# Performance work log

Measured on AMD Instinct MI355X. Metric: run time of the kernel, lower is better.

The kernel has to match this reference:

```python
import jax, jax.numpy as jnp
import numpy as np

VOCAB, D_IN, D_H = 32000, 512, 1024
B, T = 16, 256
PAD_IDX = 0


def setup_inputs() -> dict:
    key = jax.random.key(0)
    k1, k2, k3, k4, k5 = jax.random.split(key, 5)
    input_idx = jax.random.randint(k1, (B, T), 0, VOCAB, dtype=jnp.int64)
    emb = jax.random.normal(k2, (VOCAB, D_IN), dtype=jnp.float32) * 0.02
    emb = emb.at[PAD_IDX].set(0.0)  # padding_idx row is zero
    weight_x = jax.random.normal(k3, (D_H, D_IN), dtype=jnp.float32) * (1.0 / np.sqrt(D_IN))
    weight_h = jax.random.normal(k4, (D_H, D_H), dtype=jnp.float32) * (1.0 / np.sqrt(D_H))
    bias = jnp.zeros((D_H,), dtype=jnp.float32)
    lm_W = jax.random.normal(k5, (VOCAB, D_H), dtype=jnp.float32) * (1.0 / np.sqrt(D_H))
    return {"input_idx": input_idx, "emb": emb, "weight_x": weight_x,
            "weight_h": weight_h, "bias": bias, "lm_W": lm_W}


def reference(input_idx, emb, weight_x, weight_h, bias, lm_W):
    Bsz = input_idx.shape[0]
    h0 = jnp.zeros((Bsz, weight_h.shape[0]), dtype=weight_x.dtype)

    def step(h, tok):
        x = emb[tok]  # [B, D_IN]
        h_new = jnp.tanh(x @ weight_x.T + h @ weight_h.T + bias)
        mask = (tok != PAD_IDX)[:, None]  # keep old h at pad positions
        h = jnp.where(mask, h_new, h)
        return h, h

    _, h_all = jax.lax.scan(step, h0, input_idx.T)  # [T, B, H]
    h_all = jnp.swapaxes(h_all, 0, 1)               # [B, T, H]
    logits = jnp.einsum('bth,vh->btv', h_all, lm_W)  # [B, T, V]
    return logits
```

## Files before the change

### kernel.cpp

```cpp
#include <hip/hip_runtime.h>

#define PAD_IDX 0

typedef __attribute__((ext_vector_type(8))) short short8;
typedef __attribute__((ext_vector_type(4))) float f32x4;

__device__ __forceinline__ unsigned short f32_to_bf16_rne(float f) {
  unsigned int u = __builtin_bit_cast(unsigned int, f);
  u += 0x7FFFu + ((u >> 16) & 1u);
  return (unsigned short)(u >> 16);
}

__device__ __forceinline__ void load16_to_lds(const void* g, void* lds) {
  __builtin_amdgcn_global_load_lds(
      (const __attribute__((address_space(1))) unsigned int*)g,
      (__attribute__((address_space(3))) unsigned int*)lds,
      16, 0, 0);
}

__global__ void sentinel_kernel(float* out) { out[0] = 1.0e6f; }

__global__ __launch_bounds__(256) void cvt_kernel(const float* __restrict__ in,
                                                  unsigned short* __restrict__ out,
                                                  int n8) {
  int stride = gridDim.x * blockDim.x;
  for (int i = blockIdx.x * blockDim.x + threadIdx.x; i < n8; i += stride) {
    float4 a = ((const float4*)in)[2 * i];
    float4 b = ((const float4*)in)[2 * i + 1];
    ushort4 lo, hi;
    lo.x = f32_to_bf16_rne(a.x); lo.y = f32_to_bf16_rne(a.y);
    lo.z = f32_to_bf16_rne(a.z); lo.w = f32_to_bf16_rne(a.w);
    hi.x = f32_to_bf16_rne(b.x); hi.y = f32_to_bf16_rne(b.y);
    hi.z = f32_to_bf16_rne(b.z); hi.w = f32_to_bf16_rne(b.w);
    ((ushort4*)out)[2 * i] = lo;
    ((ushort4*)out)[2 * i + 1] = hi;
  }
}

__global__ __launch_bounds__(256) void xw_kernel(const int* __restrict__ tok,
                                                 const float* __restrict__ emb,
                                                 const float* __restrict__ Wx,
                                                 const float* __restrict__ bias,
                                                 float* __restrict__ xw) {
  __shared__ float At[32][68];
  __shared__ float Bt[32][68];
  __shared__ int stok[64];
  int tid = threadIdx.x;
  int tm = blockIdx.x & 63;
  int tn = blockIdx.x >> 6;
  int r0 = tm * 64, j0 = tn * 64;
  if (tid < 64) stok[tid] = tok[r0 + tid];
  int tx = tid & 15, ty = tid >> 4;
  float acc[4][4] = {};
  for (int kt = 0; kt < 512; kt += 32) {
    __syncthreads();
    #pragma unroll
    for (int ii = 0; ii < 2; ++ii) {
      int idx = tid * 2 + ii;
      int m = idx >> 3, fv = idx & 7;
      float4 va = *(const float4*)&emb[(size_t)stok[m] * 512 + kt + fv * 4];
      float4 vb = *(const float4*)&Wx[(size_t)(j0 + m) * 512 + kt + fv * 4];
      At[fv * 4 + 0][m] = va.x; At[fv * 4 + 1][m] = va.y;
      At[fv * 4 + 2][m] = va.z; At[fv * 4 + 3][m] = va.w;
      Bt[fv * 4 + 0][m] = vb.x; Bt[fv * 4 + 1][m] = vb.y;
      Bt[fv * 4 + 2][m] = vb.z; Bt[fv * 4 + 3][m] = vb.w;
    }
    __syncthreads();
    #pragma unroll
    for (int k = 0; k < 32; ++k) {
      float4 a4 = *(const float4*)&At[k][ty * 4];
      float4 b4 = *(const float4*)&Bt[k][tx * 4];
      float av[4] = {a4.x, a4.y, a4.z, a4.w};
      float bv[4] = {b4.x, b4.y, b4.z, b4.w};
      #pragma unroll
      for (int i = 0; i < 4; ++i)
        #pragma unroll
        for (int jj = 0; jj < 4; ++jj) acc[i][jj] = fmaf(av[i], bv[jj], acc[i][jj]);
    }
  }
  #pragma unroll
  for (int i = 0; i < 4; ++i) {
    size_t row = (size_t)(r0 + ty * 4 + i) * 1024 + j0 + tx * 4;
    #pragma unroll
    for (int jj = 0; jj < 4; ++jj)
      xw[row + jj] = acc[i][jj] + bias[j0 + tx * 4 + jj];
  }
}

__global__ __launch_bounds__(1024, 4) void rec_kernel(const float* __restrict__ Wh,
                                                      const float* __restrict__ xw,
                                                      const int* __restrict__ tok,
                                                      unsigned long long* hcomb,
                                                      unsigned short* __restrict__ h_all) {
  int c = blockIdx.x & 15;
  int g = blockIdx.x >> 4;
  int tid = threadIdx.x;
  int kk = tid & 15;
  int j = g * 64 + (tid >> 4);

  const float* wb = Wh + (size_t)j * 1024 + kk * 64;
#define LDW(i) f32x4 w##i = *(const f32x4*)(wb + i * 4);
  LDW(0) LDW(1) LDW(2) LDW(3) LDW(4) LDW(5) LDW(6) LDW(7)
  LDW(8) LDW(9) LDW(10) LDW(11) LDW(12) LDW(13) LDW(14) LDW(15)
#undef LDW

  __shared__ float hs[16 * 68];
  int lidx = (tid >> 6) * 68 + (tid & 63);
  unsigned long long* hc0 = hcomb + (size_t)c * 1024;
  unsigned long long* hc1 = hcomb + 16 * 1024 + (size_t)c * 1024;
  bool writer = (kk == 0);

  for (int t = 0; t < 256; ++t) {
    float xv = 0.f;
    int tkn = 1;
    if (writer) {
      xv = xw[((size_t)c * 256 + t) * 1024 + j];
      tkn = tok[c * 256 + t];
    }
    unsigned long long* src = ((t & 1) ? hc1 : hc0) + tid;
    unsigned long long v;
    int guard = 0;
    do {
      v = __hip_atomic_load(src, __ATOMIC_RELAXED, __HIP_MEMORY_SCOPE_AGENT);
      if ((unsigned int)(v >> 32) == (unsigned int)t) break;
      __builtin_amdgcn_s_sleep(1);
    } while (++guard < (1 << 20));
    hs[lidx] = __builtin_bit_cast(float, (unsigned int)v);
    __asm__ volatile("s_waitcnt lgkmcnt(0)\n\ts_barrier" ::: "memory");

    const float* hp = hs + kk * 68;
    f32x4 a0 = {0.f, 0.f, 0.f, 0.f}, a1 = a0, a2 = a0, a3 = a0;
#define FMAI(i, acc) { f32x4 h4 = *(const f32x4*)(hp + i * 4); acc += w##i * h4; }
    FMAI(0, a0) FMAI(1, a1) FMAI(2, a2) FMAI(3, a3)
    FMAI(4, a0) FMAI(5, a1) FMAI(6, a2) FMAI(7, a3)
    FMAI(8, a0) FMAI(9, a1) FMAI(10, a2) FMAI(11, a3)
    FMAI(12, a0) FMAI(13, a1) FMAI(14, a2) FMAI(15, a3)
#undef FMAI
    f32x4 aa = (a0 + a1) + (a2 + a3);
    float s = (aa[0] + aa[1]) + (aa[2] + aa[3]);
    s += __shfl_xor(s, 1);
    s += __shfl_xor(s, 2);
    s += __shfl_xor(s, 4);
    s += __shfl_xor(s, 8);

    if (writer) {
      float hnew;
      if (tkn != PAD_IDX) {
        float pre = xv + s;
        float e = __builtin_amdgcn_exp2f(pre * 2.8853900817779268f);
        hnew = 1.0f - 2.0f / (e + 1.0f);
      } else {
        hnew = hs[(j >> 6) * 68 + (j & 63)];
      }
      unsigned long long pv =
          ((unsigned long long)(unsigned int)(t + 1) << 32) |
          (unsigned long long)__builtin_bit_cast(unsigned int, hnew);
      __hip_atomic_store((((t + 1) & 1) ? hc1 : hc0) + j, pv,
                         __ATOMIC_RELAXED, __HIP_MEMORY_SCOPE_AGENT);
      h_all[((size_t)c * 256 + t) * 1024 + j] = f32_to_bf16_rne(hnew);
    }
    __asm__ volatile("s_waitcnt lgkmcnt(0)\n\ts_barrier" ::: "memory");
  }
}

__global__ __launch_bounds__(256) void gemm_kernel(const unsigned short* __restrict__ A,
                                                   const unsigned short* __restrict__ B,
                                                   float* __restrict__ C) {
  __shared__ unsigned short sA[128 * 64];
  __shared__ unsigned short sB[128 * 64];
  int tid = threadIdx.x;
  int lane = tid & 63, wave = tid >> 6;
  int id = blockIdx.x;
  int s = (id & 7) * 1000 + (id >> 3);
  int tm = s & 31, tn = s >> 5;
  int r0 = tm * 128, c0 = tn * 128;
  int wm = wave >> 1, wn = wave & 1;
  f32x4 zero = {0.f, 0.f, 0.f, 0.f};
  f32x4 acc[4][4];
  #pragma unroll
  for (int i = 0; i < 4; ++i)
    #pragma unroll
    for (int jx = 0; jx < 4; ++jx) acc[i][jx] = zero;

  for (int kt = 0; kt < 16; ++kt) {
    __syncthreads();
    #pragma unroll
    for (int i = 0; i < 4; ++i) {
      int slot = i * 256 + tid;
      int m = slot >> 3, sg = slot & 7;
      int kg = sg ^ (m & 7);
      const unsigned short* ga = A + (size_t)(r0 + m) * 1024 + kt * 64 + kg * 8;
      load16_to_lds(ga, &sA[(i * 256 + wave * 64) * 8]);
      const unsigned short* gb = B + (size_t)(c0 + m) * 1024 + kt * 64 + kg * 8;
      load16_to_lds(gb, &sB[(i * 256 + wave * 64) * 8]);
    }
    __syncthreads();
    #pragma unroll
    for (int kkb = 0; kkb < 2; ++kkb) {
      short8 af[4], bf[4];
      int kbyte = kkb * 64 + (lane >> 4) * 16;
      #pragma unroll
      for (int i = 0; i < 4; ++i) {
        int row = wm * 64 + i * 16 + (lane & 15);
        int off = row * 128 + (kbyte ^ ((row & 7) << 4));
        af[i] = *(const short8*)((const char*)sA + off);
        int rowb = wn * 64 + i * 16 + (lane & 15);
        int offb = rowb * 128 + (kbyte ^ ((rowb & 7) << 4));
        bf[i] = *(const short8*)((const char*)sB + offb);
      }
      #pragma unroll
      for (int i = 0; i < 4; ++i)
        #pragma unroll
        for (int jx = 0; jx < 4; ++jx)
          acc[i][jx] = __builtin_amdgcn_mfma_f32_16x16x32_bf16(af[i], bf[jx], acc[i][jx], 0, 0, 0);
    }
  }
  int rbase = r0 + wm * 64 + (lane >> 4) * 4;
  int cbase = c0 + wn * 64 + (lane & 15);
  #pragma unroll
  for (int i = 0; i < 4; ++i)
    #pragma unroll
    for (int jx = 0; jx < 4; ++jx)
      #pragma unroll
      for (int q = 0; q < 4; ++q)
        C[(size_t)(rbase + i * 16 + q) * 32000 + cbase + jx * 16] = acc[i][jx][q];
}

extern "C" void kernel_launch(void* const* d_in, const int* in_sizes, int n_in,
                              void* d_out, int out_size, void* d_ws, size_t ws_size,
                              hipStream_t stream) {
  const int* tok = (const int*)d_in[0];
  const float* emb = (const float*)d_in[1];
  const float* Wx = (const float*)d_in[2];
  const float* Wh = (const float*)d_in[3];
  const float* bias = (const float*)d_in[4];
  const float* lmW = (const float*)d_in[5];
  float* out = (float*)d_out;

  const size_t OFF_LMW = 0;
  const size_t OFF_XW = 65536000;
  const size_t OFF_HALL = OFF_XW + 16777216;
  const size_t OFF_HCMB = OFF_HALL + 8388608;
  const size_t NEED = OFF_HCMB + 262144;
  if (ws_size < NEED) {
    sentinel_kernel<<<1, 1, 0, stream>>>(out);
    return;
  }
  char* ws = (char*)d_ws;
  unsigned short* lmW_bf = (unsigned short*)(ws + OFF_LMW);
  float* xw = (float*)(ws + OFF_XW);
  unsigned short* h_all = (unsigned short*)(ws + OFF_HALL);
  unsigned long long* hcomb = (unsigned long long*)(ws + OFF_HCMB);

  hipMemsetAsync(ws + OFF_HCMB, 0, 262144, stream);
  cvt_kernel<<<2048, 256, 0, stream>>>(lmW, lmW_bf, 32000 * 1024 / 8);
  xw_kernel<<<1024, 256, 0, stream>>>(tok, emb, Wx, bias, xw);
  rec_kernel<<<256, 1024, 0, stream>>>(Wh, xw, tok, hcomb, h_all);
  gemm_kernel<<<8000, 256, 0, stream>>>(h_all, lmW_bf, out);
}
```

Measured before the change: 1.058 ms.

## Double-buffer recurrence LDS, busy-poll without sleep, and triple-buffer 256x128 GEMM

In the recurrence kernel, the shared hidden-state buffer is double-buffered by timestep parity. This allows removing the trailing barrier at the end of each step, and the spin loop now polls without s_sleep, cutting per-step sync latency. The logits GEMM moves to 512-thread blocks computing 256x128 tiles. It uses a three-stage LDS ring with async global-to-LDS loads two tiles ahead, vmcnt-based waits, and setprio around the MFMA block, to overlap loads with compute. Risks: more LDS per block, and hotter spinning on the atomic flags.

```diff
diff --git a/kernel.cpp b/kernel.cpp
--- a/kernel.cpp
+++ b/kernel.cpp
@@ -104,31 +104,32 @@
   LDW(8) LDW(9) LDW(10) LDW(11) LDW(12) LDW(13) LDW(14) LDW(15)
 #undef LDW
 
-  __shared__ float hs[16 * 68];
+  __shared__ float hs[2][16 * 68];
   int lidx = (tid >> 6) * 68 + (tid & 63);
   unsigned long long* hc0 = hcomb + (size_t)c * 1024;
   unsigned long long* hc1 = hcomb + 16 * 1024 + (size_t)c * 1024;
   bool writer = (kk == 0);
 
   for (int t = 0; t < 256; ++t) {
+    int p = t & 1;
     float xv = 0.f;
     int tkn = 1;
+    size_t rowoff = ((size_t)c * 256 + t) * 1024 + j;
     if (writer) {
-      xv = xw[((size_t)c * 256 + t) * 1024 + j];
+      xv = xw[rowoff];
       tkn = tok[c * 256 + t];
     }
-    unsigned long long* src = ((t & 1) ? hc1 : hc0) + tid;
+    unsigned long long* src = (p ? hc1 : hc0) + tid;
     unsigned long long v;
     int guard = 0;
     do {
       v = __hip_atomic_load(src, __ATOMIC_RELAXED, __HIP_MEMORY_SCOPE_AGENT);
       if ((unsigned int)(v >> 32) == (unsigned int)t) break;
-      __builtin_amdgcn_s_sleep(1);
-    } while (++guard < (1 << 20));
-    hs[lidx] = __builtin_bit_cast(float, (unsigned int)v);
+    } while (++guard < (1 << 22));
+    hs[p][lidx] = __builtin_bit_cast(float, (unsigned int)v);
     __asm__ volatile("s_waitcnt lgkmcnt(0)\n\ts_barrier" ::: "memory");
 
-    const float* hp = hs + kk * 68;
+    const float* hp = hs[p] + kk * 68;
     f32x4 a0 = {0.f, 0.f, 0.f, 0.f}, a1 = a0, a2 = a0, a3 = a0;
 #define FMAI(i, acc) { f32x4 h4 = *(const f32x4*)(hp + i * 4); acc += w##i * h4; }
     FMAI(0, a0) FMAI(1, a1) FMAI(2, a2) FMAI(3, a3)
@@ -150,31 +151,51 @@
         float e = __builtin_amdgcn_exp2f(pre * 2.8853900817779268f);
         hnew = 1.0f - 2.0f / (e + 1.0f);
       } else {
-        hnew = hs[(j >> 6) * 68 + (j & 63)];
+        hnew = hs[p][(j >> 6) * 68 + (j & 63)];
       }
       unsigned long long pv =
           ((unsigned long long)(unsigned int)(t + 1) << 32) |
           (unsigned long long)__builtin_bit_cast(unsigned int, hnew);
       __hip_atomic_store((((t + 1) & 1) ? hc1 : hc0) + j, pv,
                          __ATOMIC_RELAXED, __HIP_MEMORY_SCOPE_AGENT);
-      h_all[((size_t)c * 256 + t) * 1024 + j] = f32_to_bf16_rne(hnew);
-    }
-    __asm__ volatile("s_waitcnt lgkmcnt(0)\n\ts_barrier" ::: "memory");
-  }
-}
-
-__global__ __launch_bounds__(256) void gemm_kernel(const unsigned short* __restrict__ A,
+      h_all[rowoff] = f32_to_bf16_rne(hnew);
+    }
+  }
+}
+
+__global__ __launch_bounds__(512) void gemm_kernel(const unsigned short* __restrict__ A,
                                                    const unsigned short* __restrict__ B,
                                                    float* __restrict__ C) {
-  __shared__ unsigned short sA[128 * 64];
-  __shared__ unsigned short sB[128 * 64];
+  __shared__ unsigned short lds[3 * 24576];
   int tid = threadIdx.x;
   int lane = tid & 63, wave = tid >> 6;
-  int id = blockIdx.x;
-  int s = (id & 7) * 1000 + (id >> 3);
-  int tm = s & 31, tn = s >> 5;
-  int r0 = tm * 128, c0 = tn * 128;
+  int bid = blockIdx.x;
+  int wgid = (bid & 7) * 500 + (bid >> 3);
+  int tm = wgid & 15, tn = wgid >> 4;
+  int r0 = tm * 256, c0 = tn * 128;
   int wm = wave >> 1, wn = wave & 1;
+
+  auto STAGE = [&](int kt, int bi) {
+    unsigned short* bufA = (unsigned short*)lds + bi * 24576;
+    unsigned short* bufB = bufA + 16384;
+    #pragma unroll
+    for (int i = 0; i < 4; ++i) {
+      int slot = i * 512 + tid;
+      int row = slot >> 3, sg = slot & 7;
+      int kg = sg ^ (row & 7);
+      const unsigned short* ga = A + (size_t)(r0 + row) * 1024 + kt * 64 + kg * 8;
+      load16_to_lds(ga, &bufA[(i * 512 + wave * 64) * 8]);
+    }
+    #pragma unroll
+    for (int i = 0; i < 2; ++i) {
+      int slot = i * 512 + tid;
+      int row = slot >> 3, sg = slot & 7;
+      int kg = sg ^ (row & 7);
+      const unsigned short* gb = B + (size_t)(c0 + row) * 1024 + kt * 64 + kg * 8;
+      load16_to_lds(gb, &bufB[(i * 512 + wave * 64) * 8]);
+    }
+  };
+
   f32x4 zero = {0.f, 0.f, 0.f, 0.f};
   f32x4 acc[4][4];
   #pragma unroll
@@ -182,39 +203,43 @@
     #pragma unroll
     for (int jx = 0; jx < 4; ++jx) acc[i][jx] = zero;
 
+  STAGE(0, 0);
+  STAGE(1, 1);
+  __asm__ volatile("s_waitcnt vmcnt(6)\n\ts_barrier" ::: "memory");
+
   for (int kt = 0; kt < 16; ++kt) {
-    __syncthreads();
-    #pragma unroll
-    for (int i = 0; i < 4; ++i) {
-      int slot = i * 256 + tid;
-      int m = slot >> 3, sg = slot & 7;
-      int kg = sg ^ (m & 7);
-      const unsigned short* ga = A + (size_t)(r0 + m) * 1024 + kt * 64 + kg * 8;
-      load16_to_lds(ga, &sA[(i * 256 + wave * 64) * 8]);
-      const unsigned short* gb = B + (size_t)(c0 + m) * 1024 + kt * 64 + kg * 8;
-      load16_to_lds(gb, &sB[(i * 256 + wave * 64) * 8]);
-    }
-    __syncthreads();
+    int bi = kt % 3;
+    const unsigned short* bufA = (const unsigned short*)lds + bi * 24576;
+    const unsigned short* bufB = bufA + 16384;
+    {
+      int nkt = kt + 2;
+      if (nkt > 15) nkt = 15;
+      STAGE(nkt, (kt + 2) % 3);
+    }
+    short8 af[4][2], bf[4][2];
     #pragma unroll
     for (int kkb = 0; kkb < 2; ++kkb) {
-      short8 af[4], bf[4];
       int kbyte = kkb * 64 + (lane >> 4) * 16;
       #pragma unroll
       for (int i = 0; i < 4; ++i) {
-        int row = wm * 64 + i * 16 + (lane & 15);
-        int off = row * 128 + (kbyte ^ ((row & 7) << 4));
-        af[i] = *(const short8*)((const char*)sA + off);
+        int rowa = wm * 64 + i * 16 + (lane & 15);
+        af[i][kkb] = *(const short8*)((const char*)bufA + rowa * 128 + (kbyte ^ ((rowa & 7) << 4)));
         int rowb = wn * 64 + i * 16 + (lane & 15);
-        int offb = rowb * 128 + (kbyte ^ ((rowb & 7) << 4));
-        bf[i] = *(const short8*)((const char*)sB + offb);
+        bf[i][kkb] = *(const short8*)((const char*)bufB + rowb * 128 + (kbyte ^ ((rowb & 7) << 4)));
       }
+    }
+    __builtin_amdgcn_s_setprio(1);
+    #pragma unroll
+    for (int kkb = 0; kkb < 2; ++kkb)
       #pragma unroll
       for (int i = 0; i < 4; ++i)
         #pragma unroll
         for (int jx = 0; jx < 4; ++jx)
-          acc[i][jx] = __builtin_amdgcn_mfma_f32_16x16x32_bf16(af[i], bf[jx], acc[i][jx], 0, 0, 0);
-    }
-  }
+          acc[i][jx] = __builtin_amdgcn_mfma_f32_16x16x32_bf16(af[i][kkb], bf[jx][kkb], acc[i][jx], 0, 0, 0);
+    __builtin_amdgcn_s_setprio(0);
+    __asm__ volatile("s_waitcnt vmcnt(6)\n\ts_barrier" ::: "memory");
+  }
+
   int rbase = r0 + wm * 64 + (lane >> 4) * 4;
   int cbase = c0 + wn * 64 + (lane & 15);
   #pragma unroll
@@ -256,5 +281,5 @@
   cvt_kernel<<<2048, 256, 0, stream>>>(lmW, lmW_bf, 32000 * 1024 / 8);
   xw_kernel<<<1024, 256, 0, stream>>>(tok, emb, Wx, bias, xw);
   rec_kernel<<<256, 1024, 0, stream>>>(Wh, xw, tok, hcomb, h_all);
-  gemm_kernel<<<8000, 256, 0, stream>>>(h_all, lmW_bf, out);
-}
+  gemm_kernel<<<4000, 512, 0, stream>>>(h_all, lmW_bf, out);
+}
```

Measured after the change: 1.212 ms. 14.6% more time.
